# Performance work log

Hardware: AMD Instinct MI355X
Metric: run time of the kernel (lower is better)

The kernel has to match this reference:

```python
import jax, jax.numpy as jnp
import numpy as np

ACT_DIM = 768
DICT_SIZE = 32768
S0 = 4096          # top-level latent size (dict_size // prod(lower sizes))
S1 = 8             # lower_level_latent_sizes[0]
K = 64             # per-token top-k (applied globally as k * batch)


def setup_inputs() -> dict:
    key = jax.random.key(0)
    ks = jax.random.split(key, 7)
    scale_e = 1.0 / np.sqrt(ACT_DIM)
    scale_d = 1.0 / np.sqrt(DICT_SIZE)
    return {
        "x": jax.random.normal(ks[0], (4096, ACT_DIM), dtype=jnp.float32),
        "W0": jax.random.normal(ks[1], (S0, ACT_DIM), dtype=jnp.float32) * scale_e,
        "b0": jnp.zeros((S0,), dtype=jnp.float32),
        "W1": jax.random.normal(ks[2], (DICT_SIZE, ACT_DIM), dtype=jnp.float32) * scale_e,
        "b1": jnp.zeros((DICT_SIZE,), dtype=jnp.float32),
        "Wd": jax.random.normal(ks[3], (ACT_DIM, DICT_SIZE), dtype=jnp.float32) * scale_d,
        "b_dec": jnp.zeros((ACT_DIM,), dtype=jnp.float32),
    }


def reference(x, W0, b0, W1, b1, Wd, b_dec):
    B = x.shape[0]
    x_centered = x - b_dec                                   # [B, D]
    # hierarchical relu encoders
    l0 = jax.nn.relu(x_centered @ W0.T + b0)                 # [B, S0]
    l1 = jax.nn.relu(x_centered @ W1.T + b1)                 # [B, S0*S1]
    # multiplicative gating: lower-level gate broadcast over finest level
    final_dense = (l1.reshape(B, S0, S1) * l0[:, :, None]).reshape(B, S0 * S1)
    # global batch top-k over flattened [B * dict_size]
    flat = final_dense.reshape(-1)
    k_for_batch = min(K * B, flat.shape[0])
    vals, idx = jax.lax.top_k(flat, k_for_batch)
    sparse_flat = jnp.zeros_like(flat).at[idx].set(vals)
    encoded = sparse_flat.reshape(B, S0 * S1)
    # decode
    x_hat = encoded @ Wd.T + b_dec                           # [B, D]
    return x_hat
```

## Files before the change

kernel.cpp:

```cpp
#include <hip/hip_runtime.h>
#include <stdint.h>

#define DDIM 768
#define BROWS 4096
#define S0N 4096
#define DICT 32768
#define KTOT 262144u
#define PREF 2.0f
#define DELTA 4e-3f
#define CAND_CAP 8388608u
#define BAND_CAP 4096

static constexpr size_t OFF_XH   = 0;
static constexpr size_t OFF_XL   = 6291456;
static constexpr size_t OFF_W0H  = 12582912;
static constexpr size_t OFF_W0L  = 18874368;
static constexpr size_t OFF_W1H  = 25165824;
static constexpr size_t OFF_W1L  = 75497472;
static constexpr size_t OFF_WDT  = 0;
static constexpr size_t OFF_L0   = 125829120;
static constexpr size_t OFF_CTRL = 192937984;
static constexpr size_t OFF_ROWC = 193069056;
static constexpr size_t OFF_ROWD = 193085440;
static constexpr size_t OFF_CAND = 201474048;
static constexpr size_t WS_NEED  = 268582912;


typedef __attribute__((ext_vector_type(8))) short bf16x8;
typedef __attribute__((ext_vector_type(4))) float f32x4;

__device__ __forceinline__ unsigned umin_(unsigned a, unsigned b) { return a < b ? a : b; }
__device__ __forceinline__ float relu_(float v) { return v > 0.f ? v : 0.f; }

__device__ __forceinline__ unsigned short f2bf(float f) {
    union { float f; unsigned u; } v; v.f = f;
    unsigned r = v.u + 0x7FFFu + ((v.u >> 16) & 1u);
    return (unsigned short)(r >> 16);
}
__device__ __forceinline__ float bf2f(unsigned short h) {
    union { float f; unsigned u; } v; v.u = ((unsigned)h) << 16;
    return v.f;
}
__device__ __forceinline__ void split1(float a, short& h, short& l) {
    unsigned short hb = f2bf(a);
    float rem = a - bf2f(hb);
    h = (short)hb;
    l = (short)f2bf(rem);
}

__device__ __forceinline__ void gl16(const void* g, void* l) {
    __builtin_amdgcn_global_load_lds(
        (const __attribute__((address_space(1))) void*)g,
        (__attribute__((address_space(3))) void*)l,
        16, 0, 0);
}

__global__ void k_split_x(const float* __restrict__ x, const float* __restrict__ b_dec,
                          short* __restrict__ XH, short* __restrict__ XL) {
    int i = blockIdx.x * 256 + threadIdx.x;
    float4 xv = ((const float4*)x)[i];
    int d = (i % (DDIM / 4)) * 4;
    float4 bv = *(const float4*)(b_dec + d);
    float a[4] = {xv.x - bv.x, xv.y - bv.y, xv.z - bv.z, xv.w - bv.w};
    short4 h, lo;
    split1(a[0], h.x, lo.x); split1(a[1], h.y, lo.y);
    split1(a[2], h.z, lo.z); split1(a[3], h.w, lo.w);
    ((short4*)XH)[i] = h;
    ((short4*)XL)[i] = lo;
}

__global__ void k_split_w(const float* __restrict__ W, short* __restrict__ H,
                          short* __restrict__ L) {
    int i = blockIdx.x * 256 + threadIdx.x;
    float4 wv = ((const float4*)W)[i];
    short4 h, lo;
    split1(wv.x, h.x, lo.x); split1(wv.y, h.y, lo.y);
    split1(wv.z, h.z, lo.z); split1(wv.w, h.w, lo.w);
    ((short4*)H)[i] = h;
    ((short4*)L)[i] = lo;
}

__global__ void k_transpose(const float* __restrict__ Wd, unsigned short* __restrict__ WdT) {
    __shared__ float tile[32][33];
    int j0 = blockIdx.x * 32, d0 = blockIdx.y * 32;
    int tx = threadIdx.x & 31, ty = threadIdx.x >> 5;
#pragma unroll
    for (int i = 0; i < 4; ++i)
        tile[ty + i * 8][tx] = Wd[(size_t)(d0 + ty + i * 8) * DICT + j0 + tx];
    __syncthreads();
#pragma unroll
    for (int i = 0; i < 4; ++i)
        WdT[(size_t)(j0 + ty + i * 8) * DDIM + d0 + tx] = f2bf(tile[tx][ty + i * 8]);
}

template<int EPI>
__launch_bounds__(512, 2) __global__
void k_mm(const short* __restrict__ XH, const short* __restrict__ XL,
          const short* __restrict__ WH, const short* __restrict__ WL,
          const float* __restrict__ bias, float* __restrict__ l0buf,
          uint2* __restrict__ cand, unsigned* __restrict__ ctrl) {
    __shared__ __align__(16) char smem[131072];

    const int t = threadIdx.x;
    const int w = t >> 6, l = t & 63;
    const int wm = w >> 2, wn = w & 3;
    const int lr = l & 15, lk = l >> 4;

    const int nwg = gridDim.x;
    const int bid = blockIdx.x;
    const int swz = (bid & 7) * (nwg >> 3) + (bid >> 3);
    const int bm = (swz & 15) << 8;
    const int bn = (swz >> 4) << 8;

    const int a0 = 2 * w, a1 = a0 + 1;
    const unsigned aB0 = (unsigned)(bm + (a0 >> 3) * 128 + (a0 & 7) * 16 + lr) * 768u + (unsigned)(lk * 8);
    const unsigned aB1 = (unsigned)(bm + (a1 >> 3) * 128 + (a1 & 7) * 16 + lr) * 768u + (unsigned)(lk * 8);
    const unsigned bB0 = (unsigned)(bn + (a0 >> 2) * 64 + (a0 & 3) * 16 + lr) * 768u + (unsigned)(lk * 8);
    const unsigned bB1 = (unsigned)(bn + (a1 >> 2) * 64 + (a1 & 3) * 16 + lr) * 768u + (unsigned)(lk * 8);

    f32x4 acc[8][4];
#pragma unroll
    for (int i = 0; i < 8; ++i)
#pragma unroll
        for (int j = 0; j < 4; ++j) acc[i][j] = (f32x4){0.f, 0.f, 0.f, 0.f};

#pragma unroll
    for (int J = 0; J < 3; ++J) {
        const unsigned kb = (unsigned)J * 32u;
        char* dA = smem + J * 16384 + a0 * 1024;
        char* dB = smem + 65536 + J * 16384 + a0 * 1024;
        gl16(XH + aB0 + kb, dA);
        gl16(XH + aB1 + kb, dA + 1024);
        gl16(WH + bB0 + kb, dB);
        gl16(WH + bB1 + kb, dB + 1024);
    }

#pragma unroll 1
    for (int H = 0; H < 72; ++H) {
        if (H < 70)       asm volatile("s_waitcnt vmcnt(8)" ::: "memory");
        else if (H == 70) asm volatile("s_waitcnt vmcnt(4)" ::: "memory");
        else              asm volatile("s_waitcnt vmcnt(0)" ::: "memory");
        __builtin_amdgcn_s_barrier();

        const char* rA = smem + (H & 3) * 16384;
        const char* rB = smem + 65536 + (H & 3) * 16384;

        const int J = H + 3;
        const short* As = XH; const short* Bs = WH; unsigned kb = 0;
        char* dA = nullptr; char* dB = nullptr;
        const bool hj = J < 72;
        if (hj) {
            const int ktJ = J >> 1;
            if (ktJ < 12)      { As = XH; Bs = WH; kb = (unsigned)ktJ * 64u; }
            else if (ktJ < 24) { As = XH; Bs = WL; kb = (unsigned)(ktJ - 12) * 64u; }
            else               { As = XL; Bs = WH; kb = (unsigned)(ktJ - 24) * 64u; }
            kb += (unsigned)(J & 1) * 32u;
            dA = smem + (J & 3) * 16384 + a0 * 1024;
            dB = smem + 65536 + (J & 3) * 16384 + a0 * 1024;
        }

        bf16x8 bfr[4], af[4];
#pragma unroll
        for (int nj = 0; nj < 4; ++nj)
            bfr[nj] = *(const bf16x8*)(rB + (wn * 4 + nj) * 1024 + l * 16);
#pragma unroll
        for (int m2 = 0; m2 < 4; ++m2)
            af[m2] = *(const bf16x8*)(rA + (wm * 8 + m2) * 1024 + l * 16);
        if (hj) { gl16(As + aB0 + kb, dA); gl16(As + aB1 + kb, dA + 1024); }
        __builtin_amdgcn_sched_barrier(0);
        __builtin_amdgcn_s_barrier();
        asm volatile("s_waitcnt lgkmcnt(0)" ::: "memory");
        __builtin_amdgcn_sched_barrier(0);
        __builtin_amdgcn_s_setprio(1);
#pragma unroll
        for (int m2 = 0; m2 < 4; ++m2)
#pragma unroll
            for (int nj = 0; nj < 4; ++nj)
                acc[m2][nj] = __builtin_amdgcn_mfma_f32_16x16x32_bf16(
                    af[m2], bfr[nj], acc[m2][nj], 0, 0, 0);
        __builtin_amdgcn_s_setprio(0);
        __builtin_amdgcn_s_barrier();

#pragma unroll
        for (int m2 = 0; m2 < 4; ++m2)
            af[m2] = *(const bf16x8*)(rA + (wm * 8 + 4 + m2) * 1024 + l * 16);
        if (hj) { gl16(Bs + bB0 + kb, dB); gl16(Bs + bB1 + kb, dB + 1024); }
        __builtin_amdgcn_sched_barrier(0);
        __builtin_amdgcn_s_barrier();
        asm volatile("s_waitcnt lgkmcnt(0)" ::: "memory");
        __builtin_amdgcn_sched_barrier(0);
        __builtin_amdgcn_s_setprio(1);
#pragma unroll
        for (int m2 = 0; m2 < 4; ++m2)
#pragma unroll
            for (int nj = 0; nj < 4; ++nj)
                acc[4 + m2][nj] = __builtin_amdgcn_mfma_f32_16x16x32_bf16(
                    af[m2], bfr[nj], acc[4 + m2][nj], 0, 0, 0);
        __builtin_amdgcn_s_setprio(0);
        __builtin_amdgcn_s_barrier();
    }
    __syncthreads();

    if constexpr (EPI == 0) {
#pragma unroll
        for (int mi = 0; mi < 8; ++mi) {
#pragma unroll
            for (int r = 0; r < 4; ++r) {
                const int row = bm + wm * 128 + mi * 16 + lk * 4 + r;
                float* orow = l0buf + (size_t)row * S0N;
#pragma unroll
                for (int nj = 0; nj < 4; ++nj) {
                    const int col = bn + wn * 64 + nj * 16 + lr;
                    orow[col] = relu_(acc[mi][nj][r] + bias[col]);
                }
            }
        }
    } else {
        unsigned* pscan = (unsigned*)smem;
        unsigned cnt = 0;
#pragma unroll
        for (int mi = 0; mi < 8; ++mi)
#pragma unroll
            for (int nj = 0; nj < 4; ++nj)
#pragma unroll
                for (int r = 0; r < 4; ++r) {
                    const int row = bm + wm * 128 + mi * 16 + lk * 4 + r;
                    const int col = bn + wn * 64 + nj * 16 + lr;
                    float v = relu_(acc[mi][nj][r] + bias[col]);
                    v *= l0buf[(size_t)row * S0N + (col >> 3)];
                    acc[mi][nj][r] = v;
                    cnt += (v >= PREF) ? 1u : 0u;
                }
        pscan[t] = cnt;
        __syncthreads();
        for (int s = 1; s < 512; s <<= 1) {
            unsigned v2 = (t >= s) ? pscan[t - s] : 0u;
            __syncthreads();
            pscan[t] += v2;
            __syncthreads();
        }
        if (t == 511) pscan[512] = atomicAdd(&ctrl[0], pscan[511]);
        __syncthreads();
        unsigned off = pscan[512] + pscan[t] - cnt;
#pragma unroll
        for (int mi = 0; mi < 8; ++mi)
#pragma unroll
            for (int nj = 0; nj < 4; ++nj)
#pragma unroll
                for (int r = 0; r < 4; ++r) {
                    const float v = acc[mi][nj][r];
                    if (v >= PREF) {
                        const int row = bm + wm * 128 + mi * 16 + lk * 4 + r;
                        const int col = bn + wn * 64 + nj * 16 + lr;
                        if (off < CAND_CAP)
                            cand[off] = make_uint2(__float_as_uint(v),
                                                   ((unsigned)row << 15) | (unsigned)col);
                        ++off;
                    }
                }
    }
}

__global__ void k_hist1(const uint2* __restrict__ cand, unsigned* __restrict__ ctrl) {
    __shared__ unsigned h[2048];
    for (int i = threadIdx.x; i < 2048; i += 256) h[i] = 0;
    __syncthreads();
    unsigned n = umin_(ctrl[0], CAND_CAP);
    for (unsigned i = blockIdx.x * 256 + threadIdx.x; i < n; i += gridDim.x * 256)
        atomicAdd(&h[cand[i].x >> 20], 1u);
    __syncthreads();
    unsigned* hist = ctrl + 256;
    for (int i = threadIdx.x; i < 2048; i += 256)
        if (h[i]) atomicAdd(&hist[i], h[i]);
}

__global__ void k_scan1(unsigned* __restrict__ ctrl) {
    __shared__ unsigned hs[2048];
    __shared__ unsigned cs[256];
    const unsigned* h = ctrl + 256;
    int t = threadIdx.x;
    for (int i = t; i < 2048; i += 256) hs[i] = h[i];
    __syncthreads();
    unsigned s = 0;
    for (int b = 0; b < 8; ++b) s += hs[t * 8 + b];
    cs[t] = s;
    __syncthreads();
    if (t == 0) {
        unsigned cum = 0, T = 0, cb = 0;
        for (int c = 255; c >= 0; --c) {
            if (cum + cs[c] >= KTOT) {
                for (int b = c * 8 + 7; b >= c * 8; --b) {
                    cum += hs[b];
                    if (cum >= KTOT) { T = (unsigned)b; cb = cum - hs[b]; break; }
                }
                break;
            }
            cum += cs[c];
        }
        ctrl[1] = T; ctrl[2] = cb;
    }
}

__global__ void k_hist2(const uint2* __restrict__ cand, unsigned* __restrict__ ctrl) {
    unsigned n = umin_(ctrl[0], CAND_CAP);
    unsigned T = ctrl[1];
    unsigned* hist2 = ctrl + 2304;
    for (unsigned i = blockIdx.x * 256 + threadIdx.x; i < n; i += gridDim.x * 256) {
        unsigned u = cand[i].x;
        if ((u >> 20) == T) atomicAdd(&hist2[(u >> 8) & 0xFFFu], 1u);
    }
}

__global__ void k_scan2(unsigned* __restrict__ ctrl) {
    __shared__ unsigned hs[4096];
    __shared__ unsigned cs[256];
    const unsigned* h = ctrl + 2304;
    int t = threadIdx.x;
    for (int i = t; i < 4096; i += 256) hs[i] = h[i];
    __syncthreads();
    unsigned s = 0;
    for (int b = 0; b < 16; ++b) s += hs[t * 16 + b];
    cs[t] = s;
    __syncthreads();
    if (t == 0) {
        unsigned cum = ctrl[2], T2 = 0;
        for (int c = 255; c >= 0; --c) {
            if (cum + cs[c] >= KTOT) {
                for (int b = c * 16 + 15; b >= c * 16; --b) {
                    cum += hs[b];
                    if (cum >= KTOT) { T2 = (unsigned)b; break; }
                }
                break;
            }
            cum += cs[c];
        }
        ctrl[3] = (ctrl[1] << 12) | T2;
    }
}

__global__ void k_band_rows(const uint2* __restrict__ cand, unsigned* __restrict__ ctrl,
                            unsigned* __restrict__ rowc, uint2* __restrict__ rowd) {
    __shared__ unsigned lhi;
    if (threadIdx.x == 0) lhi = 0;
    __syncthreads();
    unsigned n = umin_(ctrl[0], CAND_CAP);
    unsigned H = ctrl[3];
    float lo = __uint_as_float(H << 8) - DELTA;
    float hi = __uint_as_float((H + 1u) << 8) + DELTA;
    unsigned* band_idx = ctrl + 6400;
    unsigned my = 0;
    for (unsigned i = blockIdx.x * 256 + threadIdx.x; i < n; i += gridDim.x * 256) {
        uint2 cv = cand[i];
        float v = __uint_as_float(cv.x);
        if (v > hi) {
            ++my;
            unsigned b = cv.y >> 15;
            unsigned p = atomicAdd(&rowc[b], 1u);
            if (p < 256u) rowd[(b << 8) + p] = make_uint2(cv.y & 32767u, cv.x);
        } else if (v >= lo) {
            unsigned p = atomicAdd(&ctrl[5], 1u);
            if (p < BAND_CAP) band_idx[p] = cv.y;
        }
    }
    atomicAdd(&lhi, my);
    __syncthreads();
    if (threadIdx.x == 0 && lhi) atomicAdd(&ctrl[4], lhi);
}

__global__ void k_f64(const float* __restrict__ x, const float* __restrict__ b_dec,
                      const float* __restrict__ W0, const float* __restrict__ b0,
                      const float* __restrict__ W1, const float* __restrict__ b1,
                      const unsigned* __restrict__ ctrl, double* __restrict__ band_v) {
    unsigned n = umin_(ctrl[5], BAND_CAP);
    unsigned bi = blockIdx.x;
    if (bi >= n) return;
    const unsigned* band_idx = ctrl + 6400;
    unsigned idx = band_idx[bi];
    int b = idx >> 15, j = idx & 32767, s0 = j >> 3;
    int lane = threadIdx.x;
    const float* xr = x + (size_t)b * DDIM;
    const float* w1 = W1 + (size_t)j * DDIM;
    const float* w0 = W0 + (size_t)s0 * DDIM;
    double d1 = 0.0, d0 = 0.0;
    for (int k = lane; k < DDIM; k += 64) {
        double xv = (double)xr[k] - (double)b_dec[k];
        d1 += xv * (double)w1[k];
        d0 += xv * (double)w0[k];
    }
    for (int off = 32; off; off >>= 1) {
        d1 += __shfl_down(d1, off);
        d0 += __shfl_down(d0, off);
    }
    if (lane == 0) {
        double l1v = d1 + (double)b1[j];  l1v = l1v > 0.0 ? l1v : 0.0;
        double l0v = d0 + (double)b0[s0]; l0v = l0v > 0.0 ? l0v : 0.0;
        band_v[bi] = l1v * l0v;
    }
}

__global__ void k_final(unsigned* __restrict__ ctrl, const double* __restrict__ band_v,
                        uint2* __restrict__ extra) {
    __shared__ unsigned long long skey[BAND_CAP];
    __shared__ unsigned sidx[BAND_CAP];
    int t = threadIdx.x;
    unsigned n = umin_(ctrl[5], BAND_CAP);
    const unsigned* band_idx = ctrl + 6400;
    for (int i = t; i < BAND_CAP; i += 256) {
        if ((unsigned)i < n) {
            skey[i] = (unsigned long long)__double_as_longlong(band_v[i]);
            sidx[i] = band_idx[i];
        } else {
            skey[i] = 0ull; sidx[i] = 0xFFFFFFFFu;
        }
    }
    __syncthreads();
    for (int kk = 2; kk <= BAND_CAP; kk <<= 1) {
        for (int jj = kk >> 1; jj > 0; jj >>= 1) {
            for (int i = t; i < BAND_CAP; i += 256) {
                int ixj = i ^ jj;
                if (ixj > i) {
                    unsigned long long ka = skey[i], kb = skey[ixj];
                    unsigned ia = sidx[i], ib = sidx[ixj];
                    bool ab = (ka > kb) || (ka == kb && ia < ib);
                    bool asc = ((i & kk) == 0);
                    if (asc ? !ab : ab) {
                        skey[i] = kb; skey[ixj] = ka;
                        sidx[i] = ib; sidx[ixj] = ia;
                    }
                }
            }
            __syncthreads();
        }
    }
    unsigned c_hi = ctrl[4];
    unsigned k_rem = (c_hi < KTOT) ? (KTOT - c_hi) : 0u;
    if (k_rem > n) k_rem = n;
    if (t == 0) ctrl[6] = k_rem;
    for (unsigned i = t; i < k_rem; i += 256)
        extra[i] = make_uint2(sidx[i],
                              __float_as_uint((float)__longlong_as_double((long long)skey[i])));
}

__global__ void k_rows_b(const unsigned* __restrict__ ctrl, const uint2* __restrict__ extra,
                         unsigned* __restrict__ rowc, uint2* __restrict__ rowd) {
    unsigned k_rem = ctrl[6];
    for (unsigned i = blockIdx.x * 256 + threadIdx.x; i < k_rem; i += gridDim.x * 256) {
        unsigned idx = extra[i].x;
        unsigned b = idx >> 15;
        unsigned p = atomicAdd(&rowc[b], 1u);
        if (p < 256u) rowd[(b << 8) + p] = make_uint2(idx & 32767u, extra[i].y);
    }
}

__launch_bounds__(192) __global__
void k_decode(const uint2* __restrict__ rowd, const unsigned* __restrict__ rowc,
              const unsigned short* __restrict__ WdT, const float* __restrict__ b_dec,
              float* __restrict__ out) {
    __shared__ uint2 e[256];
    int b = blockIdx.x, t = threadIdx.x;
    unsigned c = rowc[b]; if (c > 256u) c = 256u;
    for (int i = t; i < (int)c; i += 192) e[i] = rowd[(b << 8) + i];
    __syncthreads();
    float4 a = *(const float4*)(b_dec + 4 * t);
#pragma unroll 4
    for (unsigned i = 0; i < c; ++i) {
        float v = __uint_as_float(e[i].y);
        ushort4 w4 = *(const ushort4*)(WdT + (size_t)e[i].x * DDIM + 4 * t);
        a.x = fmaf(v, bf2f(w4.x), a.x);
        a.y = fmaf(v, bf2f(w4.y), a.y);
        a.z = fmaf(v, bf2f(w4.z), a.z);
        a.w = fmaf(v, bf2f(w4.w), a.w);
    }
    *(float4*)(out + (size_t)b * DDIM + 4 * t) = a;
}

extern "C" void kernel_launch(void* const* d_in, const int* in_sizes, int n_in,
                              void* d_out, int out_size, void* d_ws, size_t ws_size,
                              hipStream_t stream) {
    const float* x     = (const float*)d_in[0];
    const float* W0    = (const float*)d_in[1];
    const float* b0    = (const float*)d_in[2];
    const float* W1    = (const float*)d_in[3];
    const float* b1    = (const float*)d_in[4];
    const float* Wd    = (const float*)d_in[5];
    const float* b_dec = (const float*)d_in[6];
    float* out = (float*)d_out;

    if (ws_size < WS_NEED) {
        hipMemsetAsync(d_out, 0, (size_t)out_size * sizeof(float), stream);
        return;
    }

    char* ws = (char*)d_ws;
    short*          XH     = (short*)(ws + OFF_XH);
    short*          XL     = (short*)(ws + OFF_XL);
    short*          W0H    = (short*)(ws + OFF_W0H);
    short*          W0L    = (short*)(ws + OFF_W0L);
    short*          W1H    = (short*)(ws + OFF_W1H);
    short*          W1L    = (short*)(ws + OFF_W1L);
    unsigned short* WdT    = (unsigned short*)(ws + OFF_WDT);
    float*          l0     = (float*)(ws + OFF_L0);
    unsigned*       ctrl   = (unsigned*)(ws + OFF_CTRL);
    double*         band_v = (double*)(ws + OFF_CTRL + 65536);
    uint2*          extra  = (uint2*)(ws + OFF_CTRL + 98304);
    unsigned*       rowc   = (unsigned*)(ws + OFF_ROWC);
    uint2*          rowd   = (uint2*)(ws + OFF_ROWD);
    uint2*          cand   = (uint2*)(ws + OFF_CAND);

    hipMemsetAsync(ctrl, 0, 6400 * sizeof(unsigned), stream);
    hipMemsetAsync(rowc, 0, BROWS * sizeof(unsigned), stream);

    k_split_x<<<(BROWS * DDIM / 4) / 256, 256, 0, stream>>>(x, b_dec, XH, XL);
    k_split_w<<<(S0N * DDIM / 4) / 256, 256, 0, stream>>>(W0, W0H, W0L);
    k_split_w<<<(DICT * DDIM / 4) / 256, 256, 0, stream>>>(W1, W1H, W1L);

    k_mm<0><<<(S0N / 256) * 16, 512, 0, stream>>>(XH, XL, W0H, W0L, b0, l0, nullptr, nullptr);
    k_mm<1><<<(DICT / 256) * 16, 512, 0, stream>>>(XH, XL, W1H, W1L, b1, l0, cand, ctrl);

    k_transpose<<<dim3(DICT / 32, DDIM / 32), 256, 0, stream>>>(Wd, WdT);

    k_hist1<<<1024, 256, 0, stream>>>(cand, ctrl);
    k_scan1<<<1, 256, 0, stream>>>(ctrl);
    k_hist2<<<1024, 256, 0, stream>>>(cand, ctrl);
    k_scan2<<<1, 256, 0, stream>>>(ctrl);
    k_band_rows<<<1024, 256, 0, stream>>>(cand, ctrl, rowc, rowd);
    k_f64<<<BAND_CAP, 64, 0, stream>>>(x, b_dec, W0, b0, W1, b1, ctrl, band_v);
    k_final<<<1, 256, 0, stream>>>(ctrl, band_v, extra);
    k_rows_b<<<32, 256, 0, stream>>>(ctrl, extra, rowc, rowd);

    k_decode<<<BROWS, 192, 0, stream>>>(rowd, rowc, WdT, b_dec, out);
}
```

Baseline: 1.143 ms.

## Fuse gate GEMM into main encoder GEMM and drop l0 buffer

The separate W0 gate GEMM launch, which wrote a 64MB l0 buffer that the W1 epilogue then gathered, is folded into the main W1 GEMM. Each block computes its 256x32 gate tile alongside the main tile with extra MFMAs, using a small extra LDS slice loaded by two waves, and applies the gate from shared memory. The cost is extra LDS usage beyond 128KB, which may cut occupancy below two blocks per CU, plus recomputing the gate tile in every M-block. The bitonic sort in the final kernel is also shrunk to the next power of two of the real count, and the decode loop is unrolled further.

```diff
diff --git a/kernel.cpp b/kernel.cpp
--- a/kernel.cpp
+++ b/kernel.cpp
@@ -18,7 +18,6 @@
 static constexpr size_t OFF_W1H  = 25165824;
 static constexpr size_t OFF_W1L  = 75497472;
 static constexpr size_t OFF_WDT  = 0;
-static constexpr size_t OFF_L0   = 125829120;
 static constexpr size_t OFF_CTRL = 192937984;
 static constexpr size_t OFF_ROWC = 193069056;
 static constexpr size_t OFF_ROWD = 193085440;
@@ -93,13 +92,13 @@
         WdT[(size_t)(j0 + ty + i * 8) * DDIM + d0 + tx] = f2bf(tile[tx][ty + i * 8]);
 }
 
-template<int EPI>
 __launch_bounds__(512, 2) __global__
 void k_mm(const short* __restrict__ XH, const short* __restrict__ XL,
           const short* __restrict__ WH, const short* __restrict__ WL,
-          const float* __restrict__ bias, float* __restrict__ l0buf,
+          const short* __restrict__ GH, const short* __restrict__ GL,
+          const float* __restrict__ bias1, const float* __restrict__ bias0,
           uint2* __restrict__ cand, unsigned* __restrict__ ctrl) {
-    __shared__ __align__(16) char smem[131072];
+    __shared__ __align__(16) char smem[139264];
 
     const int t = threadIdx.x;
     const int w = t >> 6, l = t & 63;
@@ -117,12 +116,19 @@
     const unsigned aB1 = (unsigned)(bm + (a1 >> 3) * 128 + (a1 & 7) * 16 + lr) * 768u + (unsigned)(lk * 8);
     const unsigned bB0 = (unsigned)(bn + (a0 >> 2) * 64 + (a0 & 3) * 16 + lr) * 768u + (unsigned)(lk * 8);
     const unsigned bB1 = (unsigned)(bn + (a1 >> 2) * 64 + (a1 & 3) * 16 + lr) * 768u + (unsigned)(lk * 8);
+    const unsigned gB0 = (unsigned)((bn >> 3) + w * 16 + lr) * 768u + (unsigned)(lk * 8);
+    const int cg0 = (w >> 2) * 8 + (w & 3) * 2;
 
     f32x4 acc[8][4];
 #pragma unroll
     for (int i = 0; i < 8; ++i)
 #pragma unroll
         for (int j = 0; j < 4; ++j) acc[i][j] = (f32x4){0.f, 0.f, 0.f, 0.f};
+    f32x4 acc_g[2][2];
+#pragma unroll
+    for (int i = 0; i < 2; ++i)
+#pragma unroll
+        for (int j = 0; j < 2; ++j) acc_g[i][j] = (f32x4){0.f, 0.f, 0.f, 0.f};
 
 #pragma unroll
     for (int J = 0; J < 3; ++J) {
@@ -133,40 +139,55 @@
         gl16(XH + aB1 + kb, dA + 1024);
         gl16(WH + bB0 + kb, dB);
         gl16(WH + bB1 + kb, dB + 1024);
+        if (w < 2) gl16(GH + gB0 + kb, smem + 131072 + J * 2048 + w * 1024);
     }
 
 #pragma unroll 1
     for (int H = 0; H < 72; ++H) {
-        if (H < 70)       asm volatile("s_waitcnt vmcnt(8)" ::: "memory");
-        else if (H == 70) asm volatile("s_waitcnt vmcnt(4)" ::: "memory");
-        else              asm volatile("s_waitcnt vmcnt(0)" ::: "memory");
+        if (w < 2) {
+            if (H < 70)       asm volatile("s_waitcnt vmcnt(10)" ::: "memory");
+            else if (H == 70) asm volatile("s_waitcnt vmcnt(5)" ::: "memory");
+            else              asm volatile("s_waitcnt vmcnt(0)" ::: "memory");
+        } else {
+            if (H < 70)       asm volatile("s_waitcnt vmcnt(8)" ::: "memory");
+            else if (H == 70) asm volatile("s_waitcnt vmcnt(4)" ::: "memory");
+            else              asm volatile("s_waitcnt vmcnt(0)" ::: "memory");
+        }
         __builtin_amdgcn_s_barrier();
 
         const char* rA = smem + (H & 3) * 16384;
         const char* rB = smem + 65536 + (H & 3) * 16384;
+        const char* rG = smem + 131072 + (H & 3) * 2048;
 
         const int J = H + 3;
-        const short* As = XH; const short* Bs = WH; unsigned kb = 0;
-        char* dA = nullptr; char* dB = nullptr;
+        const short* As = XH; const short* Bs = WH; const short* Gs = GH; unsigned kb = 0;
+        char* dA = nullptr; char* dB = nullptr; char* dG = nullptr;
         const bool hj = J < 72;
         if (hj) {
             const int ktJ = J >> 1;
-            if (ktJ < 12)      { As = XH; Bs = WH; kb = (unsigned)ktJ * 64u; }
-            else if (ktJ < 24) { As = XH; Bs = WL; kb = (unsigned)(ktJ - 12) * 64u; }
-            else               { As = XL; Bs = WH; kb = (unsigned)(ktJ - 24) * 64u; }
+            if (ktJ < 12)      { As = XH; Bs = WH; Gs = GH; kb = (unsigned)ktJ * 64u; }
+            else if (ktJ < 24) { As = XH; Bs = WL; Gs = GL; kb = (unsigned)(ktJ - 12) * 64u; }
+            else               { As = XL; Bs = WH; Gs = GH; kb = (unsigned)(ktJ - 24) * 64u; }
             kb += (unsigned)(J & 1) * 32u;
             dA = smem + (J & 3) * 16384 + a0 * 1024;
             dB = smem + 65536 + (J & 3) * 16384 + a0 * 1024;
-        }
-
-        bf16x8 bfr[4], af[4];
+            dG = smem + 131072 + (J & 3) * 2048 + w * 1024;
+        }
+
+        bf16x8 bfr[4], af[4], bg0, bg1, ag;
 #pragma unroll
         for (int nj = 0; nj < 4; ++nj)
             bfr[nj] = *(const bf16x8*)(rB + (wn * 4 + nj) * 1024 + l * 16);
 #pragma unroll
         for (int m2 = 0; m2 < 4; ++m2)
             af[m2] = *(const bf16x8*)(rA + (wm * 8 + m2) * 1024 + l * 16);
-        if (hj) { gl16(As + aB0 + kb, dA); gl16(As + aB1 + kb, dA + 1024); }
+        bg0 = *(const bf16x8*)(rG + l * 16);
+        bg1 = *(const bf16x8*)(rG + 1024 + l * 16);
+        ag  = *(const bf16x8*)(rA + cg0 * 1024 + l * 16);
+        if (hj) {
+            gl16(As + aB0 + kb, dA); gl16(As + aB1 + kb, dA + 1024);
+            if (w < 2) gl16(Gs + gB0 + kb, dG);
+        }
         __builtin_amdgcn_sched_barrier(0);
         __builtin_amdgcn_s_barrier();
         asm volatile("s_waitcnt lgkmcnt(0)" ::: "memory");
@@ -178,12 +199,15 @@
             for (int nj = 0; nj < 4; ++nj)
                 acc[m2][nj] = __builtin_amdgcn_mfma_f32_16x16x32_bf16(
                     af[m2], bfr[nj], acc[m2][nj], 0, 0, 0);
+        acc_g[0][0] = __builtin_amdgcn_mfma_f32_16x16x32_bf16(ag, bg0, acc_g[0][0], 0, 0, 0);
+        acc_g[0][1] = __builtin_amdgcn_mfma_f32_16x16x32_bf16(ag, bg1, acc_g[0][1], 0, 0, 0);
         __builtin_amdgcn_s_setprio(0);
         __builtin_amdgcn_s_barrier();
 
 #pragma unroll
         for (int m2 = 0; m2 < 4; ++m2)
             af[m2] = *(const bf16x8*)(rA + (wm * 8 + 4 + m2) * 1024 + l * 16);
+        ag = *(const bf16x8*)(rA + (cg0 + 1) * 1024 + l * 16);
         if (hj) { gl16(Bs + bB0 + kb, dB); gl16(Bs + bB1 + kb, dB + 1024); }
         __builtin_amdgcn_sched_barrier(0);
         __builtin_amdgcn_s_barrier();
@@ -196,69 +220,69 @@
             for (int nj = 0; nj < 4; ++nj)
                 acc[4 + m2][nj] = __builtin_amdgcn_mfma_f32_16x16x32_bf16(
                     af[m2], bfr[nj], acc[4 + m2][nj], 0, 0, 0);
+        acc_g[1][0] = __builtin_amdgcn_mfma_f32_16x16x32_bf16(ag, bg0, acc_g[1][0], 0, 0, 0);
+        acc_g[1][1] = __builtin_amdgcn_mfma_f32_16x16x32_bf16(ag, bg1, acc_g[1][1], 0, 0, 0);
         __builtin_amdgcn_s_setprio(0);
         __builtin_amdgcn_s_barrier();
     }
     __syncthreads();
 
-    if constexpr (EPI == 0) {
-#pragma unroll
-        for (int mi = 0; mi < 8; ++mi) {
+    float*    gate  = (float*)smem;
+    unsigned* pscan = (unsigned*)(smem + 36864);
+    const int s0base = bn >> 3;
+#pragma unroll
+    for (int ri = 0; ri < 2; ++ri)
+#pragma unroll
+        for (int ci = 0; ci < 2; ++ci)
 #pragma unroll
             for (int r = 0; r < 4; ++r) {
-                const int row = bm + wm * 128 + mi * 16 + lk * 4 + r;
-                float* orow = l0buf + (size_t)row * S0N;
-#pragma unroll
-                for (int nj = 0; nj < 4; ++nj) {
+                const int grow = w * 32 + ri * 16 + lk * 4 + r;
+                const int gcol = ci * 16 + lr;
+                gate[grow * 33 + gcol] = relu_(acc_g[ri][ci][r] + bias0[s0base + gcol]);
+            }
+    __syncthreads();
+
+    unsigned cnt = 0;
+#pragma unroll
+    for (int mi = 0; mi < 8; ++mi)
+#pragma unroll
+        for (int nj = 0; nj < 4; ++nj)
+#pragma unroll
+            for (int r = 0; r < 4; ++r) {
+                const int lrow = wm * 128 + mi * 16 + lk * 4 + r;
+                const int lcol = wn * 64 + nj * 16 + lr;
+                float v = relu_(acc[mi][nj][r] + bias1[bn + lcol]);
+                v *= gate[lrow * 33 + (lcol >> 3)];
+                acc[mi][nj][r] = v;
+                cnt += (v >= PREF) ? 1u : 0u;
+            }
+    pscan[t] = cnt;
+    __syncthreads();
+    for (int s = 1; s < 512; s <<= 1) {
+        unsigned v2 = (t >= s) ? pscan[t - s] : 0u;
+        __syncthreads();
+        pscan[t] += v2;
+        __syncthreads();
+    }
+    if (t == 511) pscan[512] = atomicAdd(&ctrl[0], pscan[511]);
+    __syncthreads();
+    unsigned off = pscan[512] + pscan[t] - cnt;
+#pragma unroll
+    for (int mi = 0; mi < 8; ++mi)
+#pragma unroll
+        for (int nj = 0; nj < 4; ++nj)
+#pragma unroll
+            for (int r = 0; r < 4; ++r) {
+                const float v = acc[mi][nj][r];
+                if (v >= PREF) {
+                    const int row = bm + wm * 128 + mi * 16 + lk * 4 + r;
                     const int col = bn + wn * 64 + nj * 16 + lr;
-                    orow[col] = relu_(acc[mi][nj][r] + bias[col]);
+                    if (off < CAND_CAP)
+                        cand[off] = make_uint2(__float_as_uint(v),
+                                               ((unsigned)row << 15) | (unsigned)col);
+                    ++off;
                 }
             }
-        }
-    } else {
-        unsigned* pscan = (unsigned*)smem;
-        unsigned cnt = 0;
-#pragma unroll
-        for (int mi = 0; mi < 8; ++mi)
-#pragma unroll
-            for (int nj = 0; nj < 4; ++nj)
-#pragma unroll
-                for (int r = 0; r < 4; ++r) {
-                    const int row = bm + wm * 128 + mi * 16 + lk * 4 + r;
-                    const int col = bn + wn * 64 + nj * 16 + lr;
-                    float v = relu_(acc[mi][nj][r] + bias[col]);
-                    v *= l0buf[(size_t)row * S0N + (col >> 3)];
-                    acc[mi][nj][r] = v;
-                    cnt += (v >= PREF) ? 1u : 0u;
-                }
-        pscan[t] = cnt;
-        __syncthreads();
-        for (int s = 1; s < 512; s <<= 1) {
-            unsigned v2 = (t >= s) ? pscan[t - s] : 0u;
-            __syncthreads();
-            pscan[t] += v2;
-            __syncthreads();
-        }
-        if (t == 511) pscan[512] = atomicAdd(&ctrl[0], pscan[511]);
-        __syncthreads();
-        unsigned off = pscan[512] + pscan[t] - cnt;
-#pragma unroll
-        for (int mi = 0; mi < 8; ++mi)
-#pragma unroll
-            for (int nj = 0; nj < 4; ++nj)
-#pragma unroll
-                for (int r = 0; r < 4; ++r) {
-                    const float v = acc[mi][nj][r];
-                    if (v >= PREF) {
-                        const int row = bm + wm * 128 + mi * 16 + lk * 4 + r;
-                        const int col = bn + wn * 64 + nj * 16 + lr;
-                        if (off < CAND_CAP)
-                            cand[off] = make_uint2(__float_as_uint(v),
-                                                   ((unsigned)row << 15) | (unsigned)col);
-                        ++off;
-                    }
-                }
-    }
 }
 
 __global__ void k_hist1(const uint2* __restrict__ cand, unsigned* __restrict__ ctrl) {
@@ -404,9 +428,10 @@
     __shared__ unsigned sidx[BAND_CAP];
     int t = threadIdx.x;
     unsigned n = umin_(ctrl[5], BAND_CAP);
+    unsigned m = 256; while (m < n) m <<= 1;
     const unsigned* band_idx = ctrl + 6400;
-    for (int i = t; i < BAND_CAP; i += 256) {
-        if ((unsigned)i < n) {
+    for (unsigned i = t; i < m; i += 256) {
+        if (i < n) {
             skey[i] = (unsigned long long)__double_as_longlong(band_v[i]);
             sidx[i] = band_idx[i];
         } else {
@@ -414,10 +439,10 @@
         }
     }
     __syncthreads();
-    for (int kk = 2; kk <= BAND_CAP; kk <<= 1) {
-        for (int jj = kk >> 1; jj > 0; jj >>= 1) {
-            for (int i = t; i < BAND_CAP; i += 256) {
-                int ixj = i ^ jj;
+    for (unsigned kk = 2; kk <= m; kk <<= 1) {
+        for (unsigned jj = kk >> 1; jj > 0; jj >>= 1) {
+            for (unsigned i = t; i < m; i += 256) {
+                unsigned ixj = i ^ jj;
                 if (ixj > i) {
                     unsigned long long ka = skey[i], kb = skey[ixj];
                     unsigned ia = sidx[i], ib = sidx[ixj];
@@ -462,7 +487,7 @@
     for (int i = t; i < (int)c; i += 192) e[i] = rowd[(b << 8) + i];
     __syncthreads();
     float4 a = *(const float4*)(b_dec + 4 * t);
-#pragma unroll 4
+#pragma unroll 8
     for (unsigned i = 0; i < c; ++i) {
         float v = __uint_as_float(e[i].y);
         ushort4 w4 = *(const ushort4*)(WdT + (size_t)e[i].x * DDIM + 4 * t);
@@ -499,7 +524,6 @@
     short*          W1H    = (short*)(ws + OFF_W1H);
     short*          W1L    = (short*)(ws + OFF_W1L);
     unsigned short* WdT    = (unsigned short*)(ws + OFF_WDT);
-    float*          l0     = (float*)(ws + OFF_L0);
     unsigned*       ctrl   = (unsigned*)(ws + OFF_CTRL);
     double*         band_v = (double*)(ws + OFF_CTRL + 65536);
     uint2*          extra  = (uint2*)(ws + OFF_CTRL + 98304);
@@ -514,8 +538,7 @@
     k_split_w<<<(S0N * DDIM / 4) / 256, 256, 0, stream>>>(W0, W0H, W0L);
     k_split_w<<<(DICT * DDIM / 4) / 256, 256, 0, stream>>>(W1, W1H, W1L);
 
-    k_mm<0><<<(S0N / 256) * 16, 512, 0, stream>>>(XH, XL, W0H, W0L, b0, l0, nullptr, nullptr);
-    k_mm<1><<<(DICT / 256) * 16, 512, 0, stream>>>(XH, XL, W1H, W1L, b1, l0, cand, ctrl);
+    k_mm<<<(DICT / 256) * 16, 512, 0, stream>>>(XH, XL, W1H, W1L, W0H, W0L, b1, b0, cand, ctrl);
 
     k_transpose<<<dim3(DICT / 32, DDIM / 32), 256, 0, stream>>>(Wd, WdT);
 
```

Result: no change. 1.133 ms (-0.9%).
